# Kernel optimization log

Hardware: AMD Instinct MI355X
Metric: run time of the kernel (lower is better)

## Reference

```python
import jax, jax.numpy as jnp
import numpy as np

K_TOP = 10
DEPTH = 1
N_RULES = 2
N_HOPS = 2
IS_REVERSED = (False, True)


def setup_inputs() -> dict:
    key = jax.random.key(0)
    ks = jax.random.split(key, 11)
    B, E, N, F = 16, 256, 1024, 2048
    return {
        'rel': jax.random.normal(ks[0], (B, E), jnp.float32),
        'arg1': jax.random.normal(ks[1], (B, E), jnp.float32),
        'arg2': jax.random.normal(ks[2], (B, E), jnp.float32),
        'fact_rel': jax.random.normal(ks[3], (B, F, E), jnp.float32),
        'fact_arg1': jax.random.normal(ks[4], (B, F, E), jnp.float32),
        'fact_arg2': jax.random.normal(ks[5], (B, F, E), jnp.float32),
        'nb_facts': jax.random.randint(ks[6], (B,), 1, F + 1),
        'entity_embeddings': jax.random.normal(ks[7], (B, N, E), jnp.float32),
        'nb_entities': jax.random.randint(ks[8], (B,), 1, N + 1),
        'W': jax.random.normal(ks[9], (N_RULES, N_HOPS, E, E), jnp.float32) / np.sqrt(E),
        'b': jnp.zeros((N_RULES, N_HOPS, E), jnp.float32),
    }


def _kernel_scores(q, f):
    # q: [B, M, E], f: [B, F, E] -> Gaussian kernel exp(-0.5*||q-f||^2): [B, M, F]
    d = (jnp.sum(q * q, -1)[..., None] + jnp.sum(f * f, -1)[:, None, :]
         - 2.0 * jnp.einsum('bme,bfe->bmf', q, f))
    return jnp.exp(-0.5 * jnp.maximum(d, 0.0))


def kb_score(rel, arg1, arg2, fact_rel, fact_arg1, fact_arg2, nb_facts):
    # BatchNeuralKB.score: product of per-component kernels, mask padded facts, max over facts.
    B, F, E = fact_rel.shape
    M = rel.shape[0] // B
    r = rel.reshape(B, M, E); a1 = arg1.reshape(B, M, E); a2 = arg2.reshape(B, M, E)
    s = (_kernel_scores(r, fact_rel) * _kernel_scores(a1, fact_arg1)
         * _kernel_scores(a2, fact_arg2))                       # [B, M, F]
    mask = jnp.arange(F)[None, None, :] < nb_facts[:, None, None]
    s = jnp.where(mask, s, 0.0)
    return jnp.max(s, axis=-1).reshape(-1)                      # [B*M]


def prove(rel, arg1, arg2, fact_rel, fact_arg1, fact_arg2, nb_facts,
          entity_embeddings, W, b, depth):
    scores_0 = kb_score(rel, arg1, arg2, fact_rel, fact_arg1, fact_arg2, nb_facts)
    if depth == 0:
        return scores_0
    B, E = rel.shape
    N = entity_embeddings.shape[1]
    global_res = None
    for rule_idx in range(N_RULES):
        is_rev = IS_REVERSED[rule_idx]
        hop_rel_lst = [rel @ W[rule_idx, h] + b[rule_idx, h] for h in range(N_HOPS)]
        sources, scores = arg1, None
        for hop_idx, hop_rel in enumerate(hop_rel_lst, start=1):
            sources_2d = sources.reshape(-1, E)
            nb_branches = sources_2d.shape[0] // B
            hop_rel_2d = jnp.repeat(hop_rel, nb_branches, axis=0)   # [B*br, E]
            if hop_idx < N_HOPS:
                ent_rep = jnp.repeat(entity_embeddings, nb_branches, axis=0)  # [B*br, N, E]
                all_ent_2d = ent_rep.reshape(-1, E)                  # [B*br*N, E]
                new_src_2d = jnp.repeat(sources_2d, N, axis=0)       # [B*br*N, E]
                hop_rel_big = jnp.repeat(hop_rel_2d, N, axis=0)
                na1, na2 = (all_ent_2d, new_src_2d) if is_rev else (new_src_2d, all_ent_2d)
                new_scores = prove(hop_rel_big, na1, na2, fact_rel, fact_arg1,
                                   fact_arg2, nb_facts, entity_embeddings, W, b,
                                   depth - 1).reshape(-1, N)         # [B*br, N]
                k = min(K_TOP, N)
                z_scores, z_idx = jax.lax.top_k(new_scores, k)       # [B*br, k]
                z_emb = jnp.take_along_axis(ent_rep, z_idx[..., None], axis=1)  # [B*br, k, E]
                sources = z_emb.reshape(-1, E)
                z1d = z_scores.reshape(-1)
                scores = z1d if scores is None else jnp.minimum(z1d, jnp.repeat(scores, k))
            else:
                arg2_2d = jnp.repeat(arg2, nb_branches, axis=0)
                na1, na2 = (arg2_2d, sources_2d) if is_rev else (sources_2d, arg2_2d)
                z1d = prove(hop_rel_2d, na1, na2, fact_rel, fact_arg1, fact_arg2,
                            nb_facts, entity_embeddings, W, b, depth - 1)
                scores = z1d if scores is None else jnp.minimum(z1d, scores)
        res = jnp.max(scores.reshape(B, -1), axis=1)
        global_res = res if global_res is None else jnp.maximum(global_res, res)
    return jnp.maximum(scores_0, global_res)


def reference(rel, arg1, arg2, fact_rel, fact_arg1, fact_arg2, nb_facts,
              entity_embeddings, nb_entities, W, b):
    return prove(rel, arg1, arg2, fact_rel, fact_arg1, fact_arg2, nb_facts,
                 entity_embeddings, W, b, depth=DEPTH)
```

## Files before the change

kernel.cpp:

```cpp
#include <hip/hip_runtime.h>
#include <math.h>

#define E 256
#define KTOP 10
#define NY 8
#define NINF (-__builtin_huge_valf())

typedef __attribute__((ext_vector_type(4))) float f32x4;
typedef __attribute__((ext_vector_type(2))) long i64x2;

__device__ inline float wsum(float v) {
    v += __shfl_xor(v, 1, 64);
    v += __shfl_xor(v, 2, 64);
    v += __shfl_xor(v, 4, 64);
    v += __shfl_xor(v, 8, 64);
    v += __shfl_xor(v, 16, 64);
    v += __shfl_xor(v, 32, 64);
    return v;
}

__device__ inline float wmax(float v) {
    v = fmaxf(v, __shfl_xor(v, 1, 64));
    v = fmaxf(v, __shfl_xor(v, 2, 64));
    v = fmaxf(v, __shfl_xor(v, 4, 64));
    v = fmaxf(v, __shfl_xor(v, 8, 64));
    v = fmaxf(v, __shfl_xor(v, 16, 64));
    v = fmaxf(v, __shfl_xor(v, 32, 64));
    return v;
}

__device__ inline float dot4(float4 a, float4 b) {
    return a.x * b.x + a.y * b.y + a.z * b.z + a.w * b.w;
}

__device__ inline void atomicMaxF(float* addr, float v) {
    atomicMax((unsigned int*)addr, __float_as_uint(v));
}

__device__ inline unsigned char f2fp8(float x) {
    unsigned u = __float_as_uint(x);
    unsigned s = (u >> 24) & 0x80u;
    int e = (int)((u >> 23) & 0xFF) - 127;
    unsigned m = u & 0x7FFFFFu;
    if (e < -9) return (unsigned char)s;
    if (e > 8) return (unsigned char)(s | 0x7E);
    if (e >= -6) {
        unsigned mant = m >> 20;
        unsigned rest = m & 0xFFFFFu;
        if (rest > 0x80000u || (rest == 0x80000u && (mant & 1))) mant++;
        unsigned v = (((unsigned)(e + 7)) << 3) + mant;
        if (v > 0x7Eu) v = 0x7Eu;
        return (unsigned char)(s | v);
    }
    int rs = 20 + (-6 - e);
    unsigned full = 0x800000u | m;
    unsigned mant = full >> rs;
    unsigned rem = full & ((1u << rs) - 1u);
    unsigned half = 1u << (rs - 1);
    if (rem > half || (rem == half && (mant & 1))) mant++;
    if (mant >= 8u) return (unsigned char)(s | 0x08u);
    return (unsigned char)(s | mant);
}

#if defined(__has_builtin)
#if __has_builtin(__builtin_amdgcn_cvt_pk_fp8_f32)
#define HAVE_HW_FP8 1
#endif
#endif

__device__ inline unsigned pack_fp8x4(float a, float b, float c, float d) {
#ifdef HAVE_HW_FP8
    int lo = __builtin_amdgcn_cvt_pk_fp8_f32(a, b, 0, false);
    return (unsigned)__builtin_amdgcn_cvt_pk_fp8_f32(c, d, lo, true);
#else
    return (unsigned)f2fp8(a) | ((unsigned)f2fp8(b) << 8) |
           ((unsigned)f2fp8(c) << 16) | ((unsigned)f2fp8(d) << 24);
#endif
}

__device__ inline int tile_off(int e0, int col) {
    return ((e0 >> 6) << 10) + (((e0 & 31) >> 3) << 8) + (col << 4) +
           (((e0 >> 5) & 1) << 3) + (e0 & 7);
}

__global__ void k_hoprel(const float* __restrict__ rel, const float* __restrict__ arg1,
                         const float* __restrict__ arg2, const float* __restrict__ W,
                         const float* __restrict__ bias, float* __restrict__ hr,
                         float* __restrict__ nhr, float* __restrict__ nrel,
                         float* __restrict__ na1, float* __restrict__ na2, int B) {
    int b = blockIdx.x, rh = blockIdx.y;
    int j = threadIdx.x;
    __shared__ float relS[E];
    __shared__ float red[4];
    __shared__ float red2[4];
    relS[j] = rel[b * E + j];
    __syncthreads();
    const float* Wp = W + (size_t)rh * E * E;
    float acc = bias[rh * E + j];
#pragma unroll 8
    for (int e = 0; e < E; ++e) acc = fmaf(relS[e], Wp[e * E + j], acc);
    hr[((size_t)rh * B + b) * E + j] = acc;
    float s = wsum(acc * acc);
    int wave = j >> 6;
    if ((j & 63) == 0) red[wave] = s;
    float x = 0.f;
    if (rh == 0) x = relS[j];
    else if (rh == 1) x = arg1[b * E + j];
    else if (rh == 2) x = arg2[b * E + j];
    float s2 = wsum(x * x);
    if ((j & 63) == 0) red2[wave] = s2;
    __syncthreads();
    if (j == 0) {
        nhr[rh * B + b] = red[0] + red[1] + red[2] + red[3];
        if (rh < 3) {
            float nv = red2[0] + red2[1] + red2[2] + red2[3];
            (rh == 0 ? nrel : (rh == 1 ? na1 : na2))[b] = nv;
        }
    }
}

__global__ void k_prep_ent(const float* __restrict__ ent, unsigned char* __restrict__ entb,
                           unsigned char* __restrict__ entt, float* __restrict__ ne_,
                           int BN, int N) {
    int row = blockIdx.x * 4 + (threadIdx.x >> 6);
    if (row >= BN) return;
    int lane = threadIdx.x & 63;
    float4 v = ((const float4*)(ent + (size_t)row * E))[lane];
    float s = wsum(dot4(v, v));
    if (lane == 0) ne_[row] = s;
    unsigned o = pack_fp8x4(v.x, v.y, v.z, v.w);
    ((unsigned*)(entb + (size_t)row * E))[lane] = o;
    int b = row / N, n = row % N;
    size_t tbase = ((size_t)b * (N >> 4) + (n >> 4)) * 4096;
    *(unsigned*)(entt + tbase + tile_off(lane * 4, n & 15)) = o;
}

__global__ __launch_bounds__(256, 4) void k_fused(
    const float* __restrict__ rel, const float* __restrict__ arg1,
    const float* __restrict__ arg2, const float* __restrict__ frel,
    const float* __restrict__ fa1, const float* __restrict__ fa2,
    const int* __restrict__ nbf, const float* __restrict__ hr,
    const float* __restrict__ nhr, const float* __restrict__ nrel,
    const float* __restrict__ na1, const float* __restrict__ na2,
    float* __restrict__ lw1, float* __restrict__ lw2, float* __restrict__ s0log,
    float* __restrict__ nf1, float* __restrict__ nf2,
    unsigned char* __restrict__ fa1b, unsigned char* __restrict__ fa2b,
    int B, int F) {
    int b = blockIdx.y;
    int lane = threadIdx.x & 63, wave = threadIdx.x >> 6;
    int f = blockIdx.x * 4 + wave;
    size_t bf = (size_t)b * F + f;
    float4 v  = ((const float4*)(frel + bf * E))[lane];
    float4 v1 = ((const float4*)(fa1 + bf * E))[lane];
    float4 v2 = ((const float4*)(fa2 + bf * E))[lane];
    float4 qrel = ((const float4*)(rel + (size_t)b * E))[lane];
    float4 qa1  = ((const float4*)(arg1 + (size_t)b * E))[lane];
    float4 qa2  = ((const float4*)(arg2 + (size_t)b * E))[lane];
    float4 qh00 = ((const float4*)(hr + ((size_t)0 * B + b) * E))[lane];
    float4 qh01 = ((const float4*)(hr + ((size_t)1 * B + b) * E))[lane];
    float4 qh10 = ((const float4*)(hr + ((size_t)2 * B + b) * E))[lane];
    float4 qh11 = ((const float4*)(hr + ((size_t)3 * B + b) * E))[lane];
    size_t tbase = ((size_t)b * (F >> 4) + (f >> 4)) * 4096;
    int off = tile_off(lane * 4, f & 15);
    *(unsigned*)(fa1b + tbase + off) = pack_fp8x4(v1.x, v1.y, v1.z, v1.w);
    *(unsigned*)(fa2b + tbase + off) = pack_fp8x4(v2.x, v2.y, v2.z, v2.w);
    float d_rel  = wsum(dot4(v, qrel));
    float d_h00  = wsum(dot4(v, qh00));
    float d_h01  = wsum(dot4(v, qh01));
    float d_h10  = wsum(dot4(v, qh10));
    float d_h11  = wsum(dot4(v, qh11));
    float n_fr   = wsum(dot4(v, v));
    float d_a1f1 = wsum(dot4(v1, qa1));
    float d_a2f1 = wsum(dot4(v1, qa2));
    float n_f1   = wsum(dot4(v1, v1));
    float d_a1f2 = wsum(dot4(v2, qa1));
    float d_a2f2 = wsum(dot4(v2, qa2));
    float n_f2   = wsum(dot4(v2, v2));
    if (lane == 0) {
        bool msk = (f < nbf[b]);
        float rrel  = fmaxf(nrel[b] + n_fr - 2.f * d_rel, 0.f);
        float rh00  = fmaxf(nhr[0 * B + b] + n_fr - 2.f * d_h00, 0.f);
        float rh01  = fmaxf(nhr[1 * B + b] + n_fr - 2.f * d_h01, 0.f);
        float rh10  = fmaxf(nhr[2 * B + b] + n_fr - 2.f * d_h10, 0.f);
        float rh11  = fmaxf(nhr[3 * B + b] + n_fr - 2.f * d_h11, 0.f);
        float ra1f1 = fmaxf(na1[b] + n_f1 - 2.f * d_a1f1, 0.f);
        float ra2f1 = fmaxf(na2[b] + n_f1 - 2.f * d_a2f1, 0.f);
        float ra1f2 = fmaxf(na1[b] + n_f2 - 2.f * d_a1f2, 0.f);
        float ra2f2 = fmaxf(na2[b] + n_f2 - 2.f * d_a2f2, 0.f);
        nf1[bf] = n_f1;
        nf2[bf] = n_f2;
        lw1[bf]                 = msk ? -0.5f * (rh00 + ra1f1) : NINF;
        lw1[(size_t)B * F + bf] = msk ? -0.5f * (rh10 + ra1f2) : NINF;
        lw2[bf]                 = msk ? -0.5f * (rh01 + ra2f2) : NINF;
        lw2[(size_t)B * F + bf] = msk ? -0.5f * (rh11 + ra2f1) : NINF;
        s0log[bf] = msk ? -0.5f * (rrel + ra1f1 + ra2f2) : NINF;
    }
}

__global__ void k_s0red(const float* __restrict__ s0log, float* __restrict__ out,
                        int B, int F) {
    int b = blockIdx.x;
    int tid = threadIdx.x, lane = tid & 63, wave = tid >> 6;
    float m = NINF;
    for (int f = tid; f < F; f += 256) m = fmaxf(m, s0log[(size_t)b * F + f]);
    m = wmax(m);
    __shared__ float red[4];
    if (lane == 0) red[wave] = m;
    __syncthreads();
    if (tid == 0) out[b] = expf(fmaxf(fmaxf(red[0], red[1]), fmaxf(red[2], red[3])));
}

__global__ __launch_bounds__(256, 4) void k_hop1m(
    const unsigned char* __restrict__ entt, const unsigned char* __restrict__ fa1b,
    const unsigned char* __restrict__ fa2b, const float* __restrict__ nf1,
    const float* __restrict__ nf2, const float* __restrict__ ne,
    const float* __restrict__ lw1, float* __restrict__ nsc_part, int B, int N, int F) {
    int L = blockIdx.x;
    int xcd = L & 7, s = L >> 3;
    int b = ((s >> 7) << 3) | xcd;
    int inner = s & 127;
    int r = inner >> 6, nb = (inner >> 3) & 7, fs = inner & 7;
    int BR = nb * 128;
    int F0 = fs * 256;
    const unsigned char* factb = (r == 0) ? fa2b : fa1b;
    const float* nfp = ((r == 0) ? nf2 : nf1) + (size_t)b * F;
    const float* w = lw1 + ((size_t)r * B + b) * F;
    const float* nep = ne + (size_t)b * N;

    __shared__ unsigned char bT[2][4096];

    int tid = threadIdx.x, lane = tid & 63, wave = tid >> 6;
    int lr = lane & 15, lk = lane >> 4;
    int row0 = BR + wave * 32;

    const unsigned char* At = entt + (size_t)b * N * E;
    long areg[2][8];
#pragma unroll
    for (int m = 0; m < 2; ++m) {
        const unsigned char* p = At + (size_t)((row0 >> 4) + m) * 4096 + lk * 256 +
                                 lr * 16;
#pragma unroll
        for (int g = 0; g < 4; ++g) {
            i64x2 vv = *(const i64x2*)(p + g * 1024);
            areg[m][2 * g] = vv.x;
            areg[m][2 * g + 1] = vv.y;
        }
    }
    float nh[2][4];
#pragma unroll
    for (int m = 0; m < 2; ++m)
#pragma unroll
        for (int j = 0; j < 4; ++j)
            nh[m][j] = -0.5f * nep[row0 + m * 16 + lk * 4 + j];
    float lwa[16], gfa[16];
#pragma unroll
    for (int t = 0; t < 16; ++t) {
        int fcol = F0 + t * 16 + lr;
        lwa[t] = w[fcol];
        gfa[t] = fmaf(-0.5f, nfp[fcol], lwa[t]);
    }
    float vmax[2][4];
#pragma unroll
    for (int m = 0; m < 2; ++m)
#pragma unroll
        for (int j = 0; j < 4; ++j) vmax[m][j] = NINF;

    const unsigned char* Bt = factb + (size_t)b * F * E + (size_t)(F0 >> 4) * 4096;
#define STG(buf, t)                                                            \
    __builtin_amdgcn_global_load_lds(                                          \
        (const __attribute__((address_space(1))) void*)(Bt + (size_t)(t) * 4096 + \
                                                        wave * 1024 + lane * 16), \
        (__attribute__((address_space(3))) void*)&bT[buf][wave * 1024], 16, 0, 0)

    STG(0, 0);
    __syncthreads();
#pragma unroll
    for (int t = 0; t < 16; ++t) {
        int cur = t & 1;
        if (t < 15) STG(cur ^ 1, t + 1);
        long bfr[8];
#pragma unroll
        for (int g = 0; g < 4; ++g) {
            i64x2 vv = *(const i64x2*)&bT[cur][g * 1024 + lane * 16];
            bfr[2 * g] = vv.x;
            bfr[2 * g + 1] = vv.y;
        }
        f32x4 acc0 = {0.f, 0.f, 0.f, 0.f}, acc1 = {0.f, 0.f, 0.f, 0.f};
#pragma unroll
        for (int kb = 0; kb < 8; ++kb) {
            acc0 = __builtin_amdgcn_mfma_f32_16x16x32_fp8_fp8(areg[0][kb], bfr[kb],
                                                              acc0, 0, 0, 0);
            acc1 = __builtin_amdgcn_mfma_f32_16x16x32_fp8_fp8(areg[1][kb], bfr[kb],
                                                              acc1, 0, 0, 0);
        }
#pragma unroll
        for (int j = 0; j < 4; ++j) {
            vmax[0][j] = fmaxf(vmax[0][j], fminf(acc0[j] + gfa[t] + nh[0][j], lwa[t]));
            vmax[1][j] = fmaxf(vmax[1][j], fminf(acc1[j] + gfa[t] + nh[1][j], lwa[t]));
        }
        __syncthreads();
    }
#undef STG

#pragma unroll
    for (int m = 0; m < 2; ++m)
#pragma unroll
        for (int j = 0; j < 4; ++j) {
            float v = vmax[m][j];
            v = fmaxf(v, __shfl_xor(v, 1, 64));
            v = fmaxf(v, __shfl_xor(v, 2, 64));
            v = fmaxf(v, __shfl_xor(v, 4, 64));
            v = fmaxf(v, __shfl_xor(v, 8, 64));
            if (lr == 0) {
                int row = row0 + m * 16 + lk * 4 + j;
                nsc_part[(size_t)fs * (2 * (size_t)B * N) +
                         ((size_t)r * B + b) * N + row] = v;
            }
        }
}

__global__ __launch_bounds__(256) void k_topk(const float* __restrict__ nsc_part,
                                              float* __restrict__ zval,
                                              int* __restrict__ zidx, int B, int N) {
    int b = blockIdx.x, r = blockIdx.y;
    int tid = threadIdx.x, lane = tid & 63, wave = tid >> 6;
    size_t rbN = ((size_t)r * B + b) * N;
    size_t ystr = 2 * (size_t)B * N;
    const float4* p0 = (const float4*)(nsc_part + rbN) + tid;
    float4 m = *p0;
#pragma unroll
    for (int y = 1; y < NY; ++y) {
        float4 t = *(const float4*)((const float*)p0 + (size_t)y * ystr);
        m.x = fmaxf(m.x, t.x); m.y = fmaxf(m.y, t.y);
        m.z = fmaxf(m.z, t.z); m.w = fmaxf(m.w, t.w);
    }
    float v0 = expf(m.x), v1 = expf(m.y), v2 = expf(m.z), v3 = expf(m.w);
    int base = tid * 4;
    __shared__ float rv[4];
    __shared__ int ri[4];
    for (int t = 0; t < KTOP; ++t) {
        float bv = v0; int bi = base;
        if (v1 > bv) { bv = v1; bi = base + 1; }
        if (v2 > bv) { bv = v2; bi = base + 2; }
        if (v3 > bv) { bv = v3; bi = base + 3; }
#pragma unroll
        for (int off = 32; off > 0; off >>= 1) {
            float ov = __shfl_xor(bv, off, 64);
            int oi = __shfl_xor(bi, off, 64);
            if (ov > bv || (ov == bv && oi < bi)) { bv = ov; bi = oi; }
        }
        if (lane == 0) { rv[wave] = bv; ri[wave] = bi; }
        __syncthreads();
        float fb = rv[0]; int fi = ri[0];
#pragma unroll
        for (int wv = 1; wv < 4; ++wv) {
            float ov = rv[wv]; int oi = ri[wv];
            if (ov > fb || (ov == fb && oi < fi)) { fb = ov; fi = oi; }
        }
        if (tid == 0) {
            zval[((size_t)r * B + b) * KTOP + t] = fb;
            zidx[((size_t)r * B + b) * KTOP + t] = fi;
        }
        int off = fi - base;
        v0 = (off == 0) ? -2.f : v0;
        v1 = (off == 1) ? -2.f : v1;
        v2 = (off == 2) ? -2.f : v2;
        v3 = (off == 3) ? -2.f : v3;
        __syncthreads();
    }
}

__global__ __launch_bounds__(256) void k_hop2m(
    const unsigned char* __restrict__ entb, const unsigned char* __restrict__ fa1b,
    const unsigned char* __restrict__ fa2b, const float* __restrict__ nf1,
    const float* __restrict__ nf2, const float* __restrict__ ne,
    const float* __restrict__ lw2, const int* __restrict__ zidx,
    float* __restrict__ h2part, int B, int N, int F) {
    int L = blockIdx.x;
    int xcd = L & 7, s = L >> 3;
    int b = ((s >> 4) << 3) | xcd;
    int inner = s & 15;
    int r = inner >> 3, c = inner & 7;
    const unsigned char* factb = (r == 0) ? fa1b : fa2b;
    const float* nfp = ((r == 0) ? nf1 : nf2) + (size_t)b * F;
    const float* w = lw2 + ((size_t)r * B + b) * F;
    int tid = threadIdx.x, lane = tid & 63, wave = tid >> 6;
    int lr = lane & 15, lk = lane >> 4;
    __shared__ unsigned char aLds[32 * 16 * 8];
    __shared__ float snrm[16];
    for (int ci = tid; ci < 512; ci += 256) {
        int row = ci & 15, kc = ci >> 4;
        long vv = 0;
        if (row < KTOP) {
            int idx = zidx[((size_t)r * B + b) * KTOP + row];
            vv = *(const long*)(entb + ((size_t)b * N + idx) * E + kc * 8);
        }
        *(long*)&aLds[(size_t)ci * 8] = vv;
    }
    if (tid < 16) {
        float nv = 0.f;
        if (tid < KTOP) {
            int idx = zidx[((size_t)r * B + b) * KTOP + tid];
            nv = ne[(size_t)b * N + idx];
        }
        snrm[tid] = nv;
    }
    __syncthreads();
    long afr[8];
#pragma unroll
    for (int kb = 0; kb < 8; ++kb)
        afr[kb] = *(const long*)&aLds[((kb * 4 + lk) * 16 + lr) * 8];
    float nhs[4];
#pragma unroll
    for (int j = 0; j < 4; ++j) nhs[j] = -0.5f * snrm[lk * 4 + j];
    int fbase = c * (F >> 3) + wave * (F >> 5);
    float vmax[4] = {NINF, NINF, NINF, NINF};
    const unsigned char* Bb = factb + (size_t)b * F * E;
#pragma unroll
    for (int n = 0; n < 4; ++n) {
        int fcol = fbase + n * 16;
        const unsigned char* p = Bb + (size_t)(fcol >> 4) * 4096 + lk * 256 + lr * 16;
        long bfr[8];
#pragma unroll
        for (int g = 0; g < 4; ++g) {
            i64x2 vv = *(const i64x2*)(p + g * 1024);
            bfr[2 * g] = vv.x;
            bfr[2 * g + 1] = vv.y;
        }
        f32x4 acc = {0.f, 0.f, 0.f, 0.f};
#pragma unroll
        for (int kb = 0; kb < 8; ++kb)
            acc = __builtin_amdgcn_mfma_f32_16x16x32_fp8_fp8(afr[kb], bfr[kb], acc,
                                                             0, 0, 0);
        float lwf = w[fcol + lr];
        float gf = fmaf(-0.5f, nfp[fcol + lr], lwf);
#pragma unroll
        for (int j = 0; j < 4; ++j)
            vmax[j] = fmaxf(vmax[j], fminf(acc[j] + gf + nhs[j], lwf));
    }
#pragma unroll
    for (int j = 0; j < 4; ++j) {
        float v = vmax[j];
        v = fmaxf(v, __shfl_xor(v, 1, 64));
        v = fmaxf(v, __shfl_xor(v, 2, 64));
        v = fmaxf(v, __shfl_xor(v, 4, 64));
        v = fmaxf(v, __shfl_xor(v, 8, 64));
        int sidx = lk * 4 + j;
        if (lr == 0 && sidx < KTOP)
            h2part[(((size_t)r * B + b) * KTOP + sidx) * 32 + c * 4 + wave] = v;
    }
}

__global__ void k_hop2c(const float* __restrict__ h2part, const float* __restrict__ zval,
                        float* __restrict__ out, int B) {
    int i = blockIdx.x * 256 + threadIdx.x;
    int n = 2 * B * KTOP;
    if (i < n) {
        int b = (i / KTOP) % B;
        float m = NINF;
#pragma unroll
        for (int c2 = 0; c2 < 32; ++c2) m = fmaxf(m, h2part[(size_t)i * 32 + c2]);
        float sc = fminf(expf(m), zval[i]);
        atomicMaxF(&out[b], sc);
    }
}

extern "C" void kernel_launch(void* const* d_in, const int* in_sizes, int n_in,
                              void* d_out, int out_size, void* d_ws, size_t ws_size,
                              hipStream_t stream) {
    const float* rel = (const float*)d_in[0];
    const float* arg1 = (const float*)d_in[1];
    const float* arg2 = (const float*)d_in[2];
    const float* frel = (const float*)d_in[3];
    const float* fa1 = (const float*)d_in[4];
    const float* fa2 = (const float*)d_in[5];
    const int* nbf = (const int*)d_in[6];
    const float* ent = (const float*)d_in[7];
    const float* W = (const float*)d_in[9];
    const float* bias = (const float*)d_in[10];
    int B = in_sizes[0] / E;
    int F = in_sizes[3] / (B * E);
    int N = in_sizes[7] / (B * E);
    float* out = (float*)d_out;

    float* ws = (float*)d_ws;
    size_t o = 0;
    float* hr = ws + o;   o += (size_t)4 * B * E;
    float* nhr = ws + o;  o += (size_t)4 * B;
    float* nrel = ws + o; o += B;
    float* na1 = ws + o;  o += B;
    float* na2 = ws + o;  o += B * 2;
    float* nf1 = ws + o;  o += (size_t)B * F;
    float* nf2 = ws + o;  o += (size_t)B * F;
    float* ne_ = ws + o;  o += (size_t)B * N;
    float* lw1 = ws + o;  o += (size_t)2 * B * F;
    float* lw2 = ws + o;  o += (size_t)2 * B * F;
    float* zval = ws + o; o += (size_t)2 * B * KTOP;
    int* zidx = (int*)(ws + o); o += (size_t)2 * B * KTOP;
    float* s0log = ws + o; o += (size_t)B * F;
    float* h2part = ws + o; o += (size_t)2 * B * KTOP * 32;
    float* nsc_part = ws + o; o += (size_t)NY * 2 * B * N;
    unsigned char* fa1b = (unsigned char*)(ws + o); o += (size_t)B * F * E / 4;
    unsigned char* fa2b = (unsigned char*)(ws + o); o += (size_t)B * F * E / 4;
    unsigned char* entb = (unsigned char*)(ws + o); o += (size_t)B * N * E / 4;
    unsigned char* entt = (unsigned char*)(ws + o); o += (size_t)B * N * E / 4;

    k_hoprel<<<dim3(B, 4), dim3(E), 0, stream>>>(rel, arg1, arg2, W, bias, hr, nhr,
                                                 nrel, na1, na2, B);
    k_prep_ent<<<dim3((B * N + 3) / 4), dim3(256), 0, stream>>>(ent, entb, entt, ne_,
                                                                B * N, N);
    k_fused<<<dim3(F / 4, B), dim3(256), 0, stream>>>(
        rel, arg1, arg2, frel, fa1, fa2, nbf, hr, nhr, nrel, na1, na2, lw1, lw2,
        s0log, nf1, nf2, fa1b, fa2b, B, F);
    k_s0red<<<dim3(B), dim3(256), 0, stream>>>(s0log, out, B, F);
    k_hop1m<<<dim3(2048), dim3(256), 0, stream>>>(entt, fa1b, fa2b, nf1, nf2, ne_, lw1,
                                                  nsc_part, B, N, F);
    k_topk<<<dim3(B, 2), dim3(256), 0, stream>>>(nsc_part, zval, zidx, B, N);
    k_hop2m<<<dim3(256), dim3(256), 0, stream>>>(entb, fa1b, fa2b, nf1, nf2, ne_, lw2,
                                                 zidx, h2part, B, N, F);
    k_hop2c<<<dim3((2 * B * KTOP + 255) / 256), dim3(256), 0, stream>>>(h2part, zval,
                                                                        out, B);
}
```

Measured before the change: 101.1 us.

## Process 16 facts per wave with 4-lane groups in k_fused

Reassigns work in k_fused so each wave handles 16 facts, with 4 lanes per fact looping over 16 float4 chunks. The 12 full-wave shuffle reductions per fact shrink to 2-step quad reductions, and grid size drops by 16x. In exchange, global loads become strided across facts (less coalesced per instruction), query vectors are reloaded per iteration through cache, and occupancy hint is lowered to 2 blocks.

Result: slower. 141.4 us (+39.8%).

```diff
diff --git a/kernel.cpp b/kernel.cpp
--- a/kernel.cpp
+++ b/kernel.cpp
@@ -135,7 +135,7 @@
     *(unsigned*)(entt + tbase + tile_off(lane * 4, n & 15)) = o;
 }
 
-__global__ __launch_bounds__(256, 4) void k_fused(
+__global__ __launch_bounds__(256, 2) void k_fused(
     const float* __restrict__ rel, const float* __restrict__ arg1,
     const float* __restrict__ arg2, const float* __restrict__ frel,
     const float* __restrict__ fa1, const float* __restrict__ fa2,
@@ -148,52 +148,80 @@
     int B, int F) {
     int b = blockIdx.y;
     int lane = threadIdx.x & 63, wave = threadIdx.x >> 6;
-    int f = blockIdx.x * 4 + wave;
-    size_t bf = (size_t)b * F + f;
-    float4 v  = ((const float4*)(frel + bf * E))[lane];
-    float4 v1 = ((const float4*)(fa1 + bf * E))[lane];
-    float4 v2 = ((const float4*)(fa2 + bf * E))[lane];
-    float4 qrel = ((const float4*)(rel + (size_t)b * E))[lane];
-    float4 qa1  = ((const float4*)(arg1 + (size_t)b * E))[lane];
-    float4 qa2  = ((const float4*)(arg2 + (size_t)b * E))[lane];
-    float4 qh00 = ((const float4*)(hr + ((size_t)0 * B + b) * E))[lane];
-    float4 qh01 = ((const float4*)(hr + ((size_t)1 * B + b) * E))[lane];
-    float4 qh10 = ((const float4*)(hr + ((size_t)2 * B + b) * E))[lane];
-    float4 qh11 = ((const float4*)(hr + ((size_t)3 * B + b) * E))[lane];
-    size_t tbase = ((size_t)b * (F >> 4) + (f >> 4)) * 4096;
-    int off = tile_off(lane * 4, f & 15);
-    *(unsigned*)(fa1b + tbase + off) = pack_fp8x4(v1.x, v1.y, v1.z, v1.w);
-    *(unsigned*)(fa2b + tbase + off) = pack_fp8x4(v2.x, v2.y, v2.z, v2.w);
-    float d_rel  = wsum(dot4(v, qrel));
-    float d_h00  = wsum(dot4(v, qh00));
-    float d_h01  = wsum(dot4(v, qh01));
-    float d_h10  = wsum(dot4(v, qh10));
-    float d_h11  = wsum(dot4(v, qh11));
-    float n_fr   = wsum(dot4(v, v));
-    float d_a1f1 = wsum(dot4(v1, qa1));
-    float d_a2f1 = wsum(dot4(v1, qa2));
-    float n_f1   = wsum(dot4(v1, v1));
-    float d_a1f2 = wsum(dot4(v2, qa1));
-    float d_a2f2 = wsum(dot4(v2, qa2));
-    float n_f2   = wsum(dot4(v2, v2));
-    if (lane == 0) {
+    int g = lane >> 2, c = lane & 3;
+    int f0 = blockIdx.x * 64 + wave * 16;
+    int f = f0 + g;
+    size_t bfg = (size_t)b * F + f;
+    const float4* fr4 = (const float4*)(frel + bfg * E);
+    const float4* f14 = (const float4*)(fa1 + bfg * E);
+    const float4* f24 = (const float4*)(fa2 + bfg * E);
+    const float4* q0 = (const float4*)(rel + (size_t)b * E);
+    const float4* q1 = (const float4*)(arg1 + (size_t)b * E);
+    const float4* q2 = (const float4*)(arg2 + (size_t)b * E);
+    const float4* q3 = (const float4*)(hr + ((size_t)0 * B + b) * E);
+    const float4* q4 = (const float4*)(hr + ((size_t)1 * B + b) * E);
+    const float4* q5 = (const float4*)(hr + ((size_t)2 * B + b) * E);
+    const float4* q6 = (const float4*)(hr + ((size_t)3 * B + b) * E);
+    unsigned char* t1 = fa1b + ((size_t)b * (F >> 4) + (f0 >> 4)) * 4096;
+    unsigned char* t2 = fa2b + ((size_t)b * (F >> 4) + (f0 >> 4)) * 4096;
+    int base = c * 16;
+
+    float s_rel = 0.f, s_h00 = 0.f, s_h01 = 0.f, s_h10 = 0.f, s_h11 = 0.f;
+    float s_nfr = 0.f, s_a1f1 = 0.f, s_a2f1 = 0.f, s_nf1 = 0.f;
+    float s_a1f2 = 0.f, s_a2f2 = 0.f, s_nf2 = 0.f;
+#pragma unroll
+    for (int k = 0; k < 16; ++k) {
+        float4 vr = fr4[base + k];
+        float4 v1 = f14[base + k];
+        float4 v2 = f24[base + k];
+        float4 a0 = q0[base + k];
+        float4 a1 = q1[base + k];
+        float4 a2 = q2[base + k];
+        float4 a3 = q3[base + k];
+        float4 a4 = q4[base + k];
+        float4 a5 = q5[base + k];
+        float4 a6 = q6[base + k];
+        s_rel  += dot4(vr, a0);
+        s_h00  += dot4(vr, a3);
+        s_h01  += dot4(vr, a4);
+        s_h10  += dot4(vr, a5);
+        s_h11  += dot4(vr, a6);
+        s_nfr  += dot4(vr, vr);
+        s_a1f1 += dot4(v1, a1);
+        s_a2f1 += dot4(v1, a2);
+        s_nf1  += dot4(v1, v1);
+        s_a1f2 += dot4(v2, a1);
+        s_a2f2 += dot4(v2, a2);
+        s_nf2  += dot4(v2, v2);
+        int e0 = c * 64 + k * 4;
+        int off = tile_off(e0, g);
+        *(unsigned*)(t1 + off) = pack_fp8x4(v1.x, v1.y, v1.z, v1.w);
+        *(unsigned*)(t2 + off) = pack_fp8x4(v2.x, v2.y, v2.z, v2.w);
+    }
+#define QR(s)                      \
+    s += __shfl_xor(s, 1, 64);     \
+    s += __shfl_xor(s, 2, 64);
+    QR(s_rel) QR(s_h00) QR(s_h01) QR(s_h10) QR(s_h11) QR(s_nfr)
+    QR(s_a1f1) QR(s_a2f1) QR(s_nf1) QR(s_a1f2) QR(s_a2f2) QR(s_nf2)
+#undef QR
+    if (c == 0) {
         bool msk = (f < nbf[b]);
-        float rrel  = fmaxf(nrel[b] + n_fr - 2.f * d_rel, 0.f);
-        float rh00  = fmaxf(nhr[0 * B + b] + n_fr - 2.f * d_h00, 0.f);
-        float rh01  = fmaxf(nhr[1 * B + b] + n_fr - 2.f * d_h01, 0.f);
-        float rh10  = fmaxf(nhr[2 * B + b] + n_fr - 2.f * d_h10, 0.f);
-        float rh11  = fmaxf(nhr[3 * B + b] + n_fr - 2.f * d_h11, 0.f);
-        float ra1f1 = fmaxf(na1[b] + n_f1 - 2.f * d_a1f1, 0.f);
-        float ra2f1 = fmaxf(na2[b] + n_f1 - 2.f * d_a2f1, 0.f);
-        float ra1f2 = fmaxf(na1[b] + n_f2 - 2.f * d_a1f2, 0.f);
-        float ra2f2 = fmaxf(na2[b] + n_f2 - 2.f * d_a2f2, 0.f);
-        nf1[bf] = n_f1;
-        nf2[bf] = n_f2;
-        lw1[bf]                 = msk ? -0.5f * (rh00 + ra1f1) : NINF;
-        lw1[(size_t)B * F + bf] = msk ? -0.5f * (rh10 + ra1f2) : NINF;
-        lw2[bf]                 = msk ? -0.5f * (rh01 + ra2f2) : NINF;
-        lw2[(size_t)B * F + bf] = msk ? -0.5f * (rh11 + ra2f1) : NINF;
-        s0log[bf] = msk ? -0.5f * (rrel + ra1f1 + ra2f2) : NINF;
+        float rrel  = fmaxf(nrel[b] + s_nfr - 2.f * s_rel, 0.f);
+        float rh00  = fmaxf(nhr[0 * B + b] + s_nfr - 2.f * s_h00, 0.f);
+        float rh01  = fmaxf(nhr[1 * B + b] + s_nfr - 2.f * s_h01, 0.f);
+        float rh10  = fmaxf(nhr[2 * B + b] + s_nfr - 2.f * s_h10, 0.f);
+        float rh11  = fmaxf(nhr[3 * B + b] + s_nfr - 2.f * s_h11, 0.f);
+        float ra1f1 = fmaxf(na1[b] + s_nf1 - 2.f * s_a1f1, 0.f);
+        float ra2f1 = fmaxf(na2[b] + s_nf1 - 2.f * s_a2f1, 0.f);
+        float ra1f2 = fmaxf(na1[b] + s_nf2 - 2.f * s_a1f2, 0.f);
+        float ra2f2 = fmaxf(na2[b] + s_nf2 - 2.f * s_a2f2, 0.f);
+        nf1[bfg] = s_nf1;
+        nf2[bfg] = s_nf2;
+        lw1[bfg]                 = msk ? -0.5f * (rh00 + ra1f1) : NINF;
+        lw1[(size_t)B * F + bfg] = msk ? -0.5f * (rh10 + ra1f2) : NINF;
+        lw2[bfg]                 = msk ? -0.5f * (rh01 + ra2f2) : NINF;
+        lw2[(size_t)B * F + bfg] = msk ? -0.5f * (rh11 + ra2f1) : NINF;
+        s0log[bfg] = msk ? -0.5f * (rrel + ra1f1 + ra2f2) : NINF;
     }
 }
 
@@ -509,7 +537,7 @@
                                                  nrel, na1, na2, B);
     k_prep_ent<<<dim3((B * N + 3) / 4), dim3(256), 0, stream>>>(ent, entb, entt, ne_,
                                                                 B * N, N);
-    k_fused<<<dim3(F / 4, B), dim3(256), 0, stream>>>(
+    k_fused<<<dim3(F / 64, B), dim3(256), 0, stream>>>(
         rel, arg1, arg2, frel, fa1, fa2, nbf, hr, nhr, nrel, na1, na2, lw1, lw2,
         s0log, nf1, nf2, fa1b, fa2b, B, F);
     k_s0red<<<dim3(B), dim3(256), 0, stream>>>(s0log, out, B, F);
```

## Split fact scoring into fp8 cast pass and MFMA-based pairwise distance kernel

Applied to the files above, without the earlier changes.

Replaces the fused per-fact kernel, which did twelve wave-wide shuffle reductions per fact in fp32, with three pieces. A cast kernel packs frel/fa1/fa2 into tiled fp8. A tiny kernel packs the seven query vectors into an fp8 tile. A pair kernel then computes all query-fact dots and norms with fp8 MFMA 16x16x32 instructions. This removes shuffle-reduction overhead, but it adds an extra kernel launch and a second pass over the fp8 facts. Query and fact norms and dot products are now computed at fp8 precision, which can change score accuracy.

Result: no change. 99.94 us (-1.2%).

```diff
diff --git a/kernel.cpp b/kernel.cpp
--- a/kernel.cpp
+++ b/kernel.cpp
@@ -83,16 +83,12 @@
            (((e0 >> 5) & 1) << 3) + (e0 & 7);
 }
 
-__global__ void k_hoprel(const float* __restrict__ rel, const float* __restrict__ arg1,
-                         const float* __restrict__ arg2, const float* __restrict__ W,
+__global__ void k_hoprel(const float* __restrict__ rel, const float* __restrict__ W,
                          const float* __restrict__ bias, float* __restrict__ hr,
-                         float* __restrict__ nhr, float* __restrict__ nrel,
-                         float* __restrict__ na1, float* __restrict__ na2, int B) {
+                         int B) {
     int b = blockIdx.x, rh = blockIdx.y;
     int j = threadIdx.x;
     __shared__ float relS[E];
-    __shared__ float red[4];
-    __shared__ float red2[4];
     relS[j] = rel[b * E + j];
     __syncthreads();
     const float* Wp = W + (size_t)rh * E * E;
@@ -100,23 +96,6 @@
 #pragma unroll 8
     for (int e = 0; e < E; ++e) acc = fmaf(relS[e], Wp[e * E + j], acc);
     hr[((size_t)rh * B + b) * E + j] = acc;
-    float s = wsum(acc * acc);
-    int wave = j >> 6;
-    if ((j & 63) == 0) red[wave] = s;
-    float x = 0.f;
-    if (rh == 0) x = relS[j];
-    else if (rh == 1) x = arg1[b * E + j];
-    else if (rh == 2) x = arg2[b * E + j];
-    float s2 = wsum(x * x);
-    if ((j & 63) == 0) red2[wave] = s2;
-    __syncthreads();
-    if (j == 0) {
-        nhr[rh * B + b] = red[0] + red[1] + red[2] + red[3];
-        if (rh < 3) {
-            float nv = red2[0] + red2[1] + red2[2] + red2[3];
-            (rh == 0 ? nrel : (rh == 1 ? na1 : na2))[b] = nv;
-        }
-    }
 }
 
 __global__ void k_prep_ent(const float* __restrict__ ent, unsigned char* __restrict__ entb,
@@ -135,60 +114,127 @@
     *(unsigned*)(entt + tbase + tile_off(lane * 4, n & 15)) = o;
 }
 
-__global__ __launch_bounds__(256, 4) void k_fused(
+__global__ __launch_bounds__(256) void k_cast(
+    const float* __restrict__ frel, const float* __restrict__ fa1,
+    const float* __restrict__ fa2, unsigned char* __restrict__ frb,
+    unsigned char* __restrict__ fa1b, unsigned char* __restrict__ fa2b,
+    int B, int F) {
+    int row = blockIdx.x * 4 + (threadIdx.x >> 6);
+    int lane = threadIdx.x & 63;
+    int BF = B * F;
+    if (row >= 3 * BF) return;
+    int a = row / BF, rem = row - a * BF;
+    int b = rem / F, f = rem - b * F;
+    const float* src = (a == 0) ? frel : (a == 1) ? fa1 : fa2;
+    unsigned char* dst = (a == 0) ? frb : (a == 1) ? fa1b : fa2b;
+    float4 v = ((const float4*)(src + (size_t)rem * E))[lane];
+    size_t tbase = ((size_t)b * (F >> 4) + (f >> 4)) * 4096;
+    *(unsigned*)(dst + tbase + tile_off(lane * 4, f & 15)) =
+        pack_fp8x4(v.x, v.y, v.z, v.w);
+}
+
+__global__ __launch_bounds__(64) void k_prep_q(
     const float* __restrict__ rel, const float* __restrict__ arg1,
-    const float* __restrict__ arg2, const float* __restrict__ frel,
-    const float* __restrict__ fa1, const float* __restrict__ fa2,
-    const int* __restrict__ nbf, const float* __restrict__ hr,
-    const float* __restrict__ nhr, const float* __restrict__ nrel,
-    const float* __restrict__ na1, const float* __restrict__ na2,
-    float* __restrict__ lw1, float* __restrict__ lw2, float* __restrict__ s0log,
-    float* __restrict__ nf1, float* __restrict__ nf2,
-    unsigned char* __restrict__ fa1b, unsigned char* __restrict__ fa2b,
+    const float* __restrict__ arg2, const float* __restrict__ hr,
+    unsigned char* __restrict__ qt, int B) {
+    int b = blockIdx.x;
+    int lane = threadIdx.x;
+    unsigned char* t = qt + (size_t)b * 4096;
+#define ROW(q, ptr)                                                       \
+    {                                                                     \
+        float4 v = ((const float4*)(ptr))[lane];                          \
+        *(unsigned*)(t + tile_off(lane * 4, q)) =                         \
+            pack_fp8x4(v.x, v.y, v.z, v.w);                               \
+    }
+    ROW(0, rel + (size_t)b * E)
+    ROW(1, arg1 + (size_t)b * E)
+    ROW(2, arg2 + (size_t)b * E)
+    ROW(3, hr + ((size_t)0 * B + b) * E)
+    ROW(4, hr + ((size_t)1 * B + b) * E)
+    ROW(5, hr + ((size_t)2 * B + b) * E)
+    ROW(6, hr + ((size_t)3 * B + b) * E)
+#undef ROW
+#pragma unroll
+    for (int q = 7; q < 16; ++q)
+        *(unsigned*)(t + tile_off(lane * 4, q)) = 0u;
+}
+
+__global__ __launch_bounds__(256) void k_pair(
+    const unsigned char* __restrict__ qt, const unsigned char* __restrict__ frb,
+    const unsigned char* __restrict__ fa1b, const unsigned char* __restrict__ fa2b,
+    const int* __restrict__ nbf, float* __restrict__ lw1, float* __restrict__ lw2,
+    float* __restrict__ s0log, float* __restrict__ nf1, float* __restrict__ nf2,
     int B, int F) {
     int b = blockIdx.y;
     int lane = threadIdx.x & 63, wave = threadIdx.x >> 6;
-    int f = blockIdx.x * 4 + wave;
-    size_t bf = (size_t)b * F + f;
-    float4 v  = ((const float4*)(frel + bf * E))[lane];
-    float4 v1 = ((const float4*)(fa1 + bf * E))[lane];
-    float4 v2 = ((const float4*)(fa2 + bf * E))[lane];
-    float4 qrel = ((const float4*)(rel + (size_t)b * E))[lane];
-    float4 qa1  = ((const float4*)(arg1 + (size_t)b * E))[lane];
-    float4 qa2  = ((const float4*)(arg2 + (size_t)b * E))[lane];
-    float4 qh00 = ((const float4*)(hr + ((size_t)0 * B + b) * E))[lane];
-    float4 qh01 = ((const float4*)(hr + ((size_t)1 * B + b) * E))[lane];
-    float4 qh10 = ((const float4*)(hr + ((size_t)2 * B + b) * E))[lane];
-    float4 qh11 = ((const float4*)(hr + ((size_t)3 * B + b) * E))[lane];
-    size_t tbase = ((size_t)b * (F >> 4) + (f >> 4)) * 4096;
-    int off = tile_off(lane * 4, f & 15);
-    *(unsigned*)(fa1b + tbase + off) = pack_fp8x4(v1.x, v1.y, v1.z, v1.w);
-    *(unsigned*)(fa2b + tbase + off) = pack_fp8x4(v2.x, v2.y, v2.z, v2.w);
-    float d_rel  = wsum(dot4(v, qrel));
-    float d_h00  = wsum(dot4(v, qh00));
-    float d_h01  = wsum(dot4(v, qh01));
-    float d_h10  = wsum(dot4(v, qh10));
-    float d_h11  = wsum(dot4(v, qh11));
-    float n_fr   = wsum(dot4(v, v));
-    float d_a1f1 = wsum(dot4(v1, qa1));
-    float d_a2f1 = wsum(dot4(v1, qa2));
-    float n_f1   = wsum(dot4(v1, v1));
-    float d_a1f2 = wsum(dot4(v2, qa1));
-    float d_a2f2 = wsum(dot4(v2, qa2));
-    float n_f2   = wsum(dot4(v2, v2));
-    if (lane == 0) {
+    int ti = blockIdx.x * 4 + wave;
+    int f0 = ti * 16;
+    int lr = lane & 15, lk = lane >> 4;
+    const unsigned char* qp = qt + (size_t)b * 4096 + lk * 256 + lr * 16;
+    size_t tb = ((size_t)b * (F >> 4) + ti) * 4096;
+    const unsigned char* frp = frb + tb + lk * 256 + lr * 16;
+    const unsigned char* f1p = fa1b + tb + lk * 256 + lr * 16;
+    const unsigned char* f2p = fa2b + tb + lk * 256 + lr * 16;
+    long Q[8], FR[8], F1[8], F2[8];
+#pragma unroll
+    for (int g = 0; g < 4; ++g) {
+        i64x2 a = *(const i64x2*)(qp + g * 1024);
+        Q[2 * g] = a.x; Q[2 * g + 1] = a.y;
+        i64x2 c = *(const i64x2*)(frp + g * 1024);
+        FR[2 * g] = c.x; FR[2 * g + 1] = c.y;
+        i64x2 d = *(const i64x2*)(f1p + g * 1024);
+        F1[2 * g] = d.x; F1[2 * g + 1] = d.y;
+        i64x2 e2 = *(const i64x2*)(f2p + g * 1024);
+        F2[2 * g] = e2.x; F2[2 * g + 1] = e2.y;
+    }
+    f32x4 Dqq = {0.f, 0.f, 0.f, 0.f}, D1 = Dqq, D2 = Dqq, D3 = Dqq, D4 = Dqq,
+          D5 = Dqq, D6 = Dqq;
+#pragma unroll
+    for (int kb = 0; kb < 8; ++kb) {
+        Dqq = __builtin_amdgcn_mfma_f32_16x16x32_fp8_fp8(Q[kb], Q[kb], Dqq, 0, 0, 0);
+        D1 = __builtin_amdgcn_mfma_f32_16x16x32_fp8_fp8(Q[kb], FR[kb], D1, 0, 0, 0);
+        D2 = __builtin_amdgcn_mfma_f32_16x16x32_fp8_fp8(Q[kb], F1[kb], D2, 0, 0, 0);
+        D3 = __builtin_amdgcn_mfma_f32_16x16x32_fp8_fp8(Q[kb], F2[kb], D3, 0, 0, 0);
+        D4 = __builtin_amdgcn_mfma_f32_16x16x32_fp8_fp8(FR[kb], FR[kb], D4, 0, 0, 0);
+        D5 = __builtin_amdgcn_mfma_f32_16x16x32_fp8_fp8(F1[kb], F1[kb], D5, 0, 0, 0);
+        D6 = __builtin_amdgcn_mfma_f32_16x16x32_fp8_fp8(F2[kb], F2[kb], D6, 0, 0, 0);
+    }
+    __shared__ float vals[4][16][12];
+    __shared__ float qn[4][8];
+#pragma unroll
+    for (int j = 0; j < 4; ++j) {
+        int q = lk * 4 + j;
+        if (q == 0) vals[wave][lr][0] = D1[j];
+        if (q == 3) vals[wave][lr][1] = D1[j];
+        if (q == 4) vals[wave][lr][2] = D1[j];
+        if (q == 5) vals[wave][lr][3] = D1[j];
+        if (q == 6) vals[wave][lr][4] = D1[j];
+        if (q == 1) { vals[wave][lr][5] = D2[j]; vals[wave][lr][7] = D3[j]; }
+        if (q == 2) { vals[wave][lr][6] = D2[j]; vals[wave][lr][8] = D3[j]; }
+        if (q == lr) {
+            vals[wave][lr][9] = D4[j];
+            vals[wave][lr][10] = D5[j];
+            vals[wave][lr][11] = D6[j];
+            if (q < 7) qn[wave][q] = Dqq[j];
+        }
+    }
+    if (lane < 16) {
+        int f = f0 + lane;
+        size_t bf = (size_t)b * F + f;
+        const float* vv = vals[wave][lane];
+        float nfr = vv[9], n1 = vv[10], n2 = vv[11];
         bool msk = (f < nbf[b]);
-        float rrel  = fmaxf(nrel[b] + n_fr - 2.f * d_rel, 0.f);
-        float rh00  = fmaxf(nhr[0 * B + b] + n_fr - 2.f * d_h00, 0.f);
-        float rh01  = fmaxf(nhr[1 * B + b] + n_fr - 2.f * d_h01, 0.f);
-        float rh10  = fmaxf(nhr[2 * B + b] + n_fr - 2.f * d_h10, 0.f);
-        float rh11  = fmaxf(nhr[3 * B + b] + n_fr - 2.f * d_h11, 0.f);
-        float ra1f1 = fmaxf(na1[b] + n_f1 - 2.f * d_a1f1, 0.f);
-        float ra2f1 = fmaxf(na2[b] + n_f1 - 2.f * d_a2f1, 0.f);
-        float ra1f2 = fmaxf(na1[b] + n_f2 - 2.f * d_a1f2, 0.f);
-        float ra2f2 = fmaxf(na2[b] + n_f2 - 2.f * d_a2f2, 0.f);
-        nf1[bf] = n_f1;
-        nf2[bf] = n_f2;
+        float rrel  = fmaxf(qn[wave][0] + nfr - 2.f * vv[0], 0.f);
+        float rh00  = fmaxf(qn[wave][3] + nfr - 2.f * vv[1], 0.f);
+        float rh01  = fmaxf(qn[wave][4] + nfr - 2.f * vv[2], 0.f);
+        float rh10  = fmaxf(qn[wave][5] + nfr - 2.f * vv[3], 0.f);
+        float rh11  = fmaxf(qn[wave][6] + nfr - 2.f * vv[4], 0.f);
+        float ra1f1 = fmaxf(qn[wave][1] + n1 - 2.f * vv[5], 0.f);
+        float ra2f1 = fmaxf(qn[wave][2] + n1 - 2.f * vv[6], 0.f);
+        float ra1f2 = fmaxf(qn[wave][1] + n2 - 2.f * vv[7], 0.f);
+        float ra2f2 = fmaxf(qn[wave][2] + n2 - 2.f * vv[8], 0.f);
+        nf1[bf] = n1;
+        nf2[bf] = n2;
         lw1[bf]                 = msk ? -0.5f * (rh00 + ra1f1) : NINF;
         lw1[(size_t)B * F + bf] = msk ? -0.5f * (rh10 + ra1f2) : NINF;
         lw2[bf]                 = msk ? -0.5f * (rh01 + ra2f2) : NINF;
@@ -486,10 +532,6 @@
     float* ws = (float*)d_ws;
     size_t o = 0;
     float* hr = ws + o;   o += (size_t)4 * B * E;
-    float* nhr = ws + o;  o += (size_t)4 * B;
-    float* nrel = ws + o; o += B;
-    float* na1 = ws + o;  o += B;
-    float* na2 = ws + o;  o += B * 2;
     float* nf1 = ws + o;  o += (size_t)B * F;
     float* nf2 = ws + o;  o += (size_t)B * F;
     float* ne_ = ws + o;  o += (size_t)B * N;
@@ -502,16 +544,19 @@
     float* nsc_part = ws + o; o += (size_t)NY * 2 * B * N;
     unsigned char* fa1b = (unsigned char*)(ws + o); o += (size_t)B * F * E / 4;
     unsigned char* fa2b = (unsigned char*)(ws + o); o += (size_t)B * F * E / 4;
+    unsigned char* frb = (unsigned char*)(ws + o);  o += (size_t)B * F * E / 4;
     unsigned char* entb = (unsigned char*)(ws + o); o += (size_t)B * N * E / 4;
     unsigned char* entt = (unsigned char*)(ws + o); o += (size_t)B * N * E / 4;
-
-    k_hoprel<<<dim3(B, 4), dim3(E), 0, stream>>>(rel, arg1, arg2, W, bias, hr, nhr,
-                                                 nrel, na1, na2, B);
+    unsigned char* qt = (unsigned char*)(ws + o);   o += (size_t)B * 1024;
+
+    k_hoprel<<<dim3(B, 4), dim3(E), 0, stream>>>(rel, W, bias, hr, B);
     k_prep_ent<<<dim3((B * N + 3) / 4), dim3(256), 0, stream>>>(ent, entb, entt, ne_,
                                                                 B * N, N);
-    k_fused<<<dim3(F / 4, B), dim3(256), 0, stream>>>(
-        rel, arg1, arg2, frel, fa1, fa2, nbf, hr, nhr, nrel, na1, na2, lw1, lw2,
-        s0log, nf1, nf2, fa1b, fa2b, B, F);
+    k_cast<<<dim3((3 * B * F + 3) / 4), dim3(256), 0, stream>>>(frel, fa1, fa2, frb,
+                                                                fa1b, fa2b, B, F);
+    k_prep_q<<<dim3(B), dim3(64), 0, stream>>>(rel, arg1, arg2, hr, qt, B);
+    k_pair<<<dim3(F / 64, B), dim3(256), 0, stream>>>(qt, frb, fa1b, fa2b, nbf, lw1,
+                                                      lw2, s0log, nf1, nf2, B, F);
     k_s0red<<<dim3(B), dim3(256), 0, stream>>>(s0log, out, B, F);
     k_hop1m<<<dim3(2048), dim3(256), 0, stream>>>(entt, fa1b, fa2b, nf1, nf2, ne_, lw1,
                                                   nsc_part, B, N, F);
```
